# Optimization experiments

Measured on AMD Instinct MI355X. Metric: run time of the kernel, lower is better.

The kernel has to match this reference:

```python
import jax, jax.numpy as jnp
import numpy as np

B, S, D, H = 2, 2048, 1024, 16
HD = D // H  # head_dim = 64


def setup_inputs() -> dict:
    key = jax.random.key(0)
    k1, k2, k3 = jax.random.split(key, 3)
    return {
        "hidden_states": jax.random.normal(k1, (B, S, D), dtype=jnp.float32),
        "W_attn": jax.random.normal(k2, (D, 3 * D), dtype=jnp.float32) * 0.02,
        "b_attn": jnp.zeros((3 * D,), dtype=jnp.float32),
        "W_proj": jax.random.normal(k3, (D, D), dtype=jnp.float32) * 0.02,
        "b_proj": jnp.zeros((D,), dtype=jnp.float32),
    }


def reference(hidden_states, W_attn, b_attn, W_proj, b_proj):
    b, s, d = hidden_states.shape
    qkv = hidden_states @ W_attn + b_attn  # [b, s, 3d]
    q, k, v = jnp.split(qkv, 3, axis=-1)

    def split_heads(x):  # [b, s, d] -> [b, H, s, hd]
        return x.reshape(b, s, H, HD).transpose(0, 2, 1, 3)

    q, k, v = split_heads(q), split_heads(k), split_heads(v)

    # scores: [b, H, s, s]
    w = jnp.einsum("bhqd,bhkd->bhqk", q, k) / jnp.sqrt(jnp.float32(HD))
    causal = jnp.tril(jnp.ones((s, s), dtype=bool))  # [s, s]
    mask_value = jnp.finfo(w.dtype).min
    w = jnp.where(causal[None, None, :, :], w, mask_value)
    w = jax.nn.softmax(w, axis=-1)

    score = jnp.einsum("bhqk,bhkd->bhqd", w, v)  # [b, H, s, hd]
    score = score.transpose(0, 2, 1, 3).reshape(b, s, d)
    out = score @ W_proj + b_proj
    return out
```

## Files before the change

kernel.cpp:

```cpp
#include <hip/hip_runtime.h>
#include <hip/hip_bf16.h>

typedef unsigned short bf16_t;
typedef __attribute__((ext_vector_type(8))) short bf16x8;
typedef __attribute__((ext_vector_type(4))) float f32x4;

#define MFMA16(a, b, c) __builtin_amdgcn_mfma_f32_16x16x32_bf16((a), (b), (c), 0, 0, 0)

__device__ __forceinline__ bf16_t f2bf(float f) {
  union { float f; unsigned u; } v; v.f = f;
  unsigned u = v.u;
  u += 0x7FFFu + ((u >> 16) & 1u);
  return (bf16_t)(u >> 16);
}

__device__ __forceinline__ unsigned cvt_pk_bf16(float lo, float hi) {
  unsigned r;
  asm volatile("v_cvt_pk_bf16_f32 %0, %1, %2" : "=v"(r) : "v"(lo), "v"(hi));
  return r;
}

__device__ __forceinline__ void gld_lds16(const void* g, void* l) {
  __builtin_amdgcn_global_load_lds(
      (const __attribute__((address_space(1))) unsigned int*)g,
      (__attribute__((address_space(3))) unsigned int*)l, 16, 0, 0);
}

__global__ __launch_bounds__(256) void k_f32_to_bf16(const float* __restrict__ in,
                                                     bf16_t* __restrict__ out, int n8) {
  int i = blockIdx.x * 256 + threadIdx.x;
  if (i >= n8) return;
  const float4* p = (const float4*)in + (size_t)i * 2;
  float4 a = p[0], b = p[1];
  bf16x8 o;
  o[0] = (short)f2bf(a.x); o[1] = (short)f2bf(a.y); o[2] = (short)f2bf(a.z); o[3] = (short)f2bf(a.w);
  o[4] = (short)f2bf(b.x); o[5] = (short)f2bf(b.y); o[6] = (short)f2bf(b.z); o[7] = (short)f2bf(b.w);
  *((bf16x8*)out + i) = o;
}

__global__ __launch_bounds__(256) void k_transpose_bf16(const float* __restrict__ W,
                                                        bf16_t* __restrict__ Wt, int K, int N) {
  __shared__ bf16_t t[64][65];
  int n0 = blockIdx.x * 64, k0 = blockIdx.y * 64;
  int tid = threadIdx.x;
#pragma unroll
  for (int p = 0; p < 16; ++p) {
    int lin = p * 256 + tid;
    int r = lin >> 6, c = lin & 63;
    t[r][c] = f2bf(W[(size_t)(k0 + r) * N + n0 + c]);
  }
  __syncthreads();
#pragma unroll
  for (int p = 0; p < 16; ++p) {
    int lin = p * 256 + tid;
    int nr = lin >> 6, kc = lin & 63;
    Wt[(size_t)(n0 + nr) * K + k0 + kc] = t[kc][nr];
  }
}

template <bool BF16OUT, bool SCALEQ>
__global__ __launch_bounds__(256) void k_gemm_bt(const bf16_t* __restrict__ A,
                                                 const bf16_t* __restrict__ Bt,
                                                 const float* __restrict__ bias,
                                                 void* __restrict__ Cout, int M, int N, int K,
                                                 int nx) {
  __shared__ bf16_t Al[128 * 32];
  __shared__ bf16_t Bl[128 * 32];
  const int tid = threadIdx.x;
  const int lane = tid & 63;
  const int wid = tid >> 6;
  const int wm = wid >> 1, wn = wid & 1;
  const int nwg = gridDim.x;
  const int cpx = nwg >> 3;
  const int swz = (blockIdx.x & 7) * cpx + (blockIdx.x >> 3);
  const int m0 = (swz / nx) * 128, n0 = (swz % nx) * 128;
  const int lr = lane & 15;
  const int lk = lane >> 4;

  f32x4 acc[4][4] = {};

  for (int k0 = 0; k0 < K; k0 += 32) {
    __syncthreads();
#pragma unroll
    for (int p = 0; p < 2; ++p) {
      int o = p * 4096 + tid * 16;
      int row = o >> 6, cb = o & 63;
      gld_lds16((const char*)A + ((size_t)(m0 + row) * K + k0) * 2 + cb, (char*)Al + o);
      gld_lds16((const char*)Bt + ((size_t)(n0 + row) * K + k0) * 2 + cb, (char*)Bl + o);
    }
    __syncthreads();
    bf16x8 af[4], bfr[4];
#pragma unroll
    for (int i = 0; i < 4; ++i) {
      af[i]  = *(const bf16x8*)(Al + ((wm * 64 + i * 16 + lr) * 32 + lk * 8));
      bfr[i] = *(const bf16x8*)(Bl + ((wn * 64 + i * 16 + lr) * 32 + lk * 8));
    }
#pragma unroll
    for (int i = 0; i < 4; ++i)
#pragma unroll
      for (int j = 0; j < 4; ++j)
        acc[i][j] = MFMA16(af[i], bfr[j], acc[i][j]);
  }

#pragma unroll
  for (int i = 0; i < 4; ++i) {
    int grow = m0 + wm * 64 + i * 16 + lk * 4;
#pragma unroll
    for (int j = 0; j < 4; ++j) {
      int gcol = n0 + wn * 64 + j * 16 + lr;
      float bv = bias[gcol];
      float scl = (SCALEQ && gcol < 1024) ? 0.18033688011112042f : 1.0f;
#pragma unroll
      for (int r = 0; r < 4; ++r) {
        float v = (acc[i][j][r] + bv) * scl;
        size_t off = (size_t)(grow + r) * N + gcol;
        if (BF16OUT)
          ((bf16_t*)Cout)[off] = f2bf(v);
        else
          ((float*)Cout)[off] = v;
      }
    }
  }
}

__global__ __launch_bounds__(256) void k_attn(const bf16_t* __restrict__ qkv,
                                              bf16_t* __restrict__ score) {
  __shared__ bf16_t Kl[2][64 * 64];
  __shared__ bf16_t Vt[2][64 * 64];
  __shared__ bf16_t Pl[4][16 * 64];
  const int tid = threadIdx.x;
  const int lane = tid & 63;
  const int w = tid >> 6;
  const int lr = lane & 15, lk = lane >> 4;

  const int flat = blockIdx.x;
  const int qt = 31 - (flat >> 5);
  const int bh = flat & 31;
  const int b = bh >> 4, h = bh & 15;

  const bf16_t* Qb = qkv + (size_t)b * 2048 * 3072 + h * 64;
  const bf16_t* Kb = Qb + 1024;
  const bf16_t* Vb = Qb + 2048;

  int vkv[2], vd0[2], krow[2], kchk[2];
#pragma unroll
  for (int p = 0; p < 2; ++p) {
    int e = (p * 256 + tid) * 8;
    vkv[p] = e >> 6;
    vd0[p] = e & 63;
    int t2 = p * 256 + tid;
    krow[p] = t2 >> 3;
    kchk[p] = (t2 & 7) ^ (krow[p] & 7);
  }

  const int qr0 = qt * 64 + w * 16;
  const int q = qr0 + lr;
  const int jtEnd = qt + 1;

  bf16x8 qf[2];
#pragma unroll
  for (int ks = 0; ks < 2; ++ks)
    qf[ks] = *(const bf16x8*)(Qb + (size_t)(qr0 + lr) * 3072 + ks * 32 + lk * 8);

  f32x4 o[4] = {};
  float l = 0.f;

  {
    bf16x8 v0[2];
#pragma unroll
    for (int p = 0; p < 2; ++p)
      v0[p] = *(const bf16x8*)(Vb + (size_t)vkv[p] * 3072 + vd0[p]);
#pragma unroll
    for (int p = 0; p < 2; ++p)
#pragma unroll
      for (int j = 0; j < 8; ++j) {
        int d = vd0[p] + j;
        int addr = (d * 128 + vkv[p] * 2) ^ (((d & 7) ^ ((d >> 3) & 7)) << 4);
        *(bf16_t*)((char*)Vt + addr) = (bf16_t)v0[p][j];
      }
  }
  bf16x8 vrA[2], vrB[2];
#pragma unroll
  for (int p = 0; p < 2; ++p)
    vrA[p] = *(const bf16x8*)(Vb + (size_t)(64 + vkv[p]) * 3072 + vd0[p]);
#pragma unroll
  for (int p = 0; p < 2; ++p)
    gld_lds16((const char*)Kb + ((size_t)krow[p] * 3072 + kchk[p] * 8) * 2,
              (char*)Kl + (p * 256 + tid) * 16);

  auto STEP = [&](int jt, bf16x8 (&vrC)[2], bf16x8 (&vrN)[2], bool last) {
    const int kv0 = jt * 64;
    asm volatile("s_waitcnt lgkmcnt(0)" ::: "memory");
    __builtin_amdgcn_s_barrier();
    char* wbase = (char*)Vt + (((jt + 1) & 1) << 13);
#pragma unroll
    for (int p = 0; p < 2; ++p)
#pragma unroll
      for (int j = 0; j < 8; ++j) {
        int d = vd0[p] + j;
        int addr = (d * 128 + vkv[p] * 2) ^ (((d & 7) ^ ((d >> 3) & 7)) << 4);
        *(bf16_t*)(wbase + addr) = (bf16_t)vrC[p][j];
      }
    if (!last) {
      const int kvV = (kv0 + 128 < 2048) ? kv0 + 128 : 1920;
#pragma unroll
      for (int p = 0; p < 2; ++p)
        vrN[p] = *(const bf16x8*)(Vb + (size_t)(kvV + vkv[p]) * 3072 + vd0[p]);
      char* kbase = (char*)Kl + (((jt + 1) & 1) << 13);
#pragma unroll
      for (int p = 0; p < 2; ++p)
        gld_lds16((const char*)Kb + ((size_t)(kv0 + 64 + krow[p]) * 3072 + kchk[p] * 8) * 2,
                  kbase + (p * 256 + tid) * 16);
      asm volatile("s_waitcnt vmcnt(4)" ::: "memory");
    } else {
      asm volatile("s_waitcnt vmcnt(0)" ::: "memory");
    }
    const char* kread = (const char*)Kl + ((jt & 1) << 13);
    bf16x8 kf[4][2];
#pragma unroll
    for (int nc = 0; nc < 4; ++nc) {
      const char* rowp = kread + (nc * 16 + lr) * 128;
      kf[nc][0] = *(const bf16x8*)(rowp + ((lk ^ (lr & 7)) << 4));
      kf[nc][1] = *(const bf16x8*)(rowp + (((4 | lk) ^ (lr & 7)) << 4));
    }
    f32x4 s[4];
    __builtin_amdgcn_s_setprio(1);
#pragma unroll
    for (int nc = 0; nc < 4; ++nc) {
      f32x4 z = {};
      z = MFMA16(kf[nc][0], qf[0], z);
      z = MFMA16(kf[nc][1], qf[1], z);
      s[nc] = z;
    }
    __builtin_amdgcn_s_setprio(0);
    if (kv0 + 63 > qr0) {
#pragma unroll
      for (int nc = 0; nc < 4; ++nc)
#pragma unroll
        for (int r = 0; r < 4; ++r) {
          int kvi = kv0 + nc * 16 + lk * 4 + r;
          if (kvi > q) s[nc][r] = -INFINITY;
        }
    }
#pragma unroll
    for (int nc = 0; nc < 4; ++nc)
#pragma unroll
      for (int r = 0; r < 4; ++r) {
        float p = exp2f(s[nc][r]);
        s[nc][r] = p;
        l += p;
      }
    bf16_t* Pw = Pl[w];
#pragma unroll
    for (int nc = 0; nc < 4; ++nc)
#pragma unroll
      for (int r = 0; r < 4; r += 2) {
        unsigned u = cvt_pk_bf16(s[nc][r], s[nc][r + 1]);
        int addr = (lr * 128 + (nc * 16 + lk * 4 + r) * 2) ^ ((lr & 7) << 4);
        *(unsigned*)((char*)Pw + addr) = u;
      }
    const char* rbase = (const char*)Vt + ((jt & 1) << 13);
    bf16x8 pa[2];
#pragma unroll
    for (int ks = 0; ks < 2; ++ks) {
      int addr = (lr * 128 + ks * 64 + lk * 16) ^ ((lr & 7) << 4);
      pa[ks] = *(const bf16x8*)((const char*)Pl[w] + addr);
    }
    __builtin_amdgcn_s_setprio(1);
#pragma unroll
    for (int db = 0; db < 4; ++db)
#pragma unroll
      for (int ks = 0; ks < 2; ++ks) {
        int d = db * 16 + lr;
        int addr = (d * 128 + ks * 64 + lk * 16) ^ (((d & 7) ^ ((d >> 3) & 7)) << 4);
        bf16x8 vb = *(const bf16x8*)(rbase + addr);
        o[db] = MFMA16(vb, pa[ks], o[db]);
      }
    __builtin_amdgcn_s_setprio(0);
  };

  int jt = 0;
  for (;;) {
    STEP(jt, vrA, vrB, jt + 1 == jtEnd);
    if (++jt == jtEnd) break;
    STEP(jt, vrB, vrA, jt + 1 == jtEnd);
    if (++jt == jtEnd) break;
  }

  l += __shfl_xor(l, 16);
  l += __shfl_xor(l, 32);
  const float rl = 1.0f / l;
  bf16_t* orow = score + (size_t)(b * 2048 + q) * 1024 + h * 64 + lk * 4;
#pragma unroll
  for (int db = 0; db < 4; ++db) {
    unsigned w0 = cvt_pk_bf16(o[db][0] * rl, o[db][1] * rl);
    unsigned w1 = cvt_pk_bf16(o[db][2] * rl, o[db][3] * rl);
    uint2 pkt; pkt.x = w0; pkt.y = w1;
    *(uint2*)(orow + db * 16) = pkt;
  }
}

extern "C" void kernel_launch(void* const* d_in, const int* in_sizes, int n_in,
                              void* d_out, int out_size, void* d_ws, size_t ws_size,
                              hipStream_t stream) {
  const float* X  = (const float*)d_in[0];
  const float* Wa = (const float*)d_in[1];
  const float* ba = (const float*)d_in[2];
  const float* Wp = (const float*)d_in[3];
  const float* bp = (const float*)d_in[4];
  float* out = (float*)d_out;

  char* ws = (char*)d_ws;
  bf16_t* Xb  = (bf16_t*)ws;
  bf16_t* WaT = (bf16_t*)(ws + (size_t)(8u << 20));
  bf16_t* WpT = (bf16_t*)(ws + (size_t)(14u << 20));
  bf16_t* QKV = (bf16_t*)(ws + (size_t)(16u << 20));
  bf16_t* S_  = Xb;

  k_f32_to_bf16<<<2048, 256, 0, stream>>>(X, Xb, 4096 * 1024 / 8);
  k_transpose_bf16<<<dim3(48, 16), 256, 0, stream>>>(Wa, WaT, 1024, 3072);
  k_transpose_bf16<<<dim3(16, 16), 256, 0, stream>>>(Wp, WpT, 1024, 1024);
  k_gemm_bt<true, true><<<768, 256, 0, stream>>>(Xb, WaT, ba, QKV, 4096, 3072, 1024, 24);
  k_attn<<<1024, 256, 0, stream>>>(QKV, S_);
  k_gemm_bt<false, false><<<256, 256, 0, stream>>>(S_, WpT, bp, out, 4096, 1024, 1024, 8);
}
```

Measured before the change: 124.2 us.

## Narrow output-projection GEMM tiles and vectorize V transpose and P stores

The GEMM kernel now takes the N-tile width as a template parameter. The output projection uses 128x64 tiles over 512 workgroups instead of 256, so more of the GPU's compute units have work. In the attention kernel, each thread now loads V as two 4-element rows and writes packed 32-bit pairs into the transposed LDS buffer instead of 16-bit scalar writes, and the vmcnt wait is adjusted to match. P tile stores are also combined into 64-bit writes. Narrower GEMM tiles reload the A tile more often and give each workgroup less work to reuse it against.

```diff
diff --git a/kernel.cpp b/kernel.cpp
--- a/kernel.cpp
+++ b/kernel.cpp
@@ -3,6 +3,7 @@
 
 typedef unsigned short bf16_t;
 typedef __attribute__((ext_vector_type(8))) short bf16x8;
+typedef __attribute__((ext_vector_type(4))) short bf16x4;
 typedef __attribute__((ext_vector_type(4))) float f32x4;
 
 #define MFMA16(a, b, c) __builtin_amdgcn_mfma_f32_16x16x32_bf16((a), (b), (c), 0, 0, 0)
@@ -18,6 +19,10 @@
   unsigned r;
   asm volatile("v_cvt_pk_bf16_f32 %0, %1, %2" : "=v"(r) : "v"(lo), "v"(hi));
   return r;
+}
+
+__device__ __forceinline__ unsigned pack2(short lo, short hi) {
+  return ((unsigned)(unsigned short)lo) | ((unsigned)(unsigned short)hi << 16);
 }
 
 __device__ __forceinline__ void gld_lds16(const void* g, void* l) {
@@ -58,14 +63,15 @@
   }
 }
 
-template <bool BF16OUT, bool SCALEQ>
+template <bool BF16OUT, bool SCALEQ, int BN>
 __global__ __launch_bounds__(256) void k_gemm_bt(const bf16_t* __restrict__ A,
                                                  const bf16_t* __restrict__ Bt,
                                                  const float* __restrict__ bias,
                                                  void* __restrict__ Cout, int M, int N, int K,
                                                  int nx) {
+  constexpr int NJ = BN / 32;
   __shared__ bf16_t Al[128 * 32];
-  __shared__ bf16_t Bl[128 * 32];
+  __shared__ bf16_t Bl[BN * 32];
   const int tid = threadIdx.x;
   const int lane = tid & 63;
   const int wid = tid >> 6;
@@ -73,11 +79,11 @@
   const int nwg = gridDim.x;
   const int cpx = nwg >> 3;
   const int swz = (blockIdx.x & 7) * cpx + (blockIdx.x >> 3);
-  const int m0 = (swz / nx) * 128, n0 = (swz % nx) * 128;
+  const int m0 = (swz / nx) * 128, n0 = (swz % nx) * BN;
   const int lr = lane & 15;
   const int lk = lane >> 4;
 
-  f32x4 acc[4][4] = {};
+  f32x4 acc[4][NJ] = {};
 
   for (int k0 = 0; k0 < K; k0 += 32) {
     __syncthreads();
@@ -86,19 +92,25 @@
       int o = p * 4096 + tid * 16;
       int row = o >> 6, cb = o & 63;
       gld_lds16((const char*)A + ((size_t)(m0 + row) * K + k0) * 2 + cb, (char*)Al + o);
+    }
+#pragma unroll
+    for (int p = 0; p < BN / 64; ++p) {
+      int o = p * 4096 + tid * 16;
+      int row = o >> 6, cb = o & 63;
       gld_lds16((const char*)Bt + ((size_t)(n0 + row) * K + k0) * 2 + cb, (char*)Bl + o);
     }
     __syncthreads();
-    bf16x8 af[4], bfr[4];
-#pragma unroll
-    for (int i = 0; i < 4; ++i) {
-      af[i]  = *(const bf16x8*)(Al + ((wm * 64 + i * 16 + lr) * 32 + lk * 8));
-      bfr[i] = *(const bf16x8*)(Bl + ((wn * 64 + i * 16 + lr) * 32 + lk * 8));
-    }
+    bf16x8 af[4], bfr[NJ];
 #pragma unroll
     for (int i = 0; i < 4; ++i)
-#pragma unroll
-      for (int j = 0; j < 4; ++j)
+      af[i] = *(const bf16x8*)(Al + ((wm * 64 + i * 16 + lr) * 32 + lk * 8));
+#pragma unroll
+    for (int j = 0; j < NJ; ++j)
+      bfr[j] = *(const bf16x8*)(Bl + ((wn * (BN / 2) + j * 16 + lr) * 32 + lk * 8));
+#pragma unroll
+    for (int i = 0; i < 4; ++i)
+#pragma unroll
+      for (int j = 0; j < NJ; ++j)
         acc[i][j] = MFMA16(af[i], bfr[j], acc[i][j]);
   }
 
@@ -106,8 +118,8 @@
   for (int i = 0; i < 4; ++i) {
     int grow = m0 + wm * 64 + i * 16 + lk * 4;
 #pragma unroll
-    for (int j = 0; j < 4; ++j) {
-      int gcol = n0 + wn * 64 + j * 16 + lr;
+    for (int j = 0; j < NJ; ++j) {
+      int gcol = n0 + wn * (BN / 2) + j * 16 + lr;
       float bv = bias[gcol];
       float scl = (SCALEQ && gcol < 1024) ? 0.18033688011112042f : 1.0f;
 #pragma unroll
@@ -142,15 +154,14 @@
   const bf16_t* Kb = Qb + 1024;
   const bf16_t* Vb = Qb + 2048;
 
-  int vkv[2], vd0[2], krow[2], kchk[2];
+  int d0c[2], kv2[2], krow[2], kchk[2];
 #pragma unroll
   for (int p = 0; p < 2; ++p) {
-    int e = (p * 256 + tid) * 8;
-    vkv[p] = e >> 6;
-    vd0[p] = e & 63;
-    int t2 = p * 256 + tid;
-    krow[p] = t2 >> 3;
-    kchk[p] = (t2 & 7) ^ (krow[p] & 7);
+    int e = p * 256 + tid;
+    d0c[p] = (e & 15) * 4;
+    kv2[p] = (e >> 4) * 2;
+    krow[p] = e >> 3;
+    kchk[p] = (e & 7) ^ (krow[p] & 7);
   }
 
   const int qr0 = qt * 64 + w * 16;
@@ -166,29 +177,33 @@
   float l = 0.f;
 
   {
-    bf16x8 v0[2];
+    bf16x4 v0[2][2];
+#pragma unroll
+    for (int p = 0; p < 2; ++p) {
+      v0[p][0] = *(const bf16x4*)(Vb + (size_t)kv2[p] * 3072 + d0c[p]);
+      v0[p][1] = *(const bf16x4*)(Vb + (size_t)(kv2[p] + 1) * 3072 + d0c[p]);
+    }
 #pragma unroll
     for (int p = 0; p < 2; ++p)
-      v0[p] = *(const bf16x8*)(Vb + (size_t)vkv[p] * 3072 + vd0[p]);
-#pragma unroll
-    for (int p = 0; p < 2; ++p)
-#pragma unroll
-      for (int j = 0; j < 8; ++j) {
-        int d = vd0[p] + j;
-        int addr = (d * 128 + vkv[p] * 2) ^ (((d & 7) ^ ((d >> 3) & 7)) << 4);
-        *(bf16_t*)((char*)Vt + addr) = (bf16_t)v0[p][j];
-      }
-  }
-  bf16x8 vrA[2], vrB[2];
-#pragma unroll
-  for (int p = 0; p < 2; ++p)
-    vrA[p] = *(const bf16x8*)(Vb + (size_t)(64 + vkv[p]) * 3072 + vd0[p]);
+#pragma unroll
+      for (int j = 0; j < 4; ++j) {
+        int d = d0c[p] + j;
+        int addr = (d * 128 + kv2[p] * 2) ^ (((d & 7) ^ ((d >> 3) & 7)) << 4);
+        *(unsigned*)((char*)Vt + addr) = pack2(v0[p][0][j], v0[p][1][j]);
+      }
+  }
+  bf16x4 vrA[2][2], vrB[2][2];
+#pragma unroll
+  for (int p = 0; p < 2; ++p) {
+    vrA[p][0] = *(const bf16x4*)(Vb + (size_t)(64 + kv2[p]) * 3072 + d0c[p]);
+    vrA[p][1] = *(const bf16x4*)(Vb + (size_t)(64 + kv2[p] + 1) * 3072 + d0c[p]);
+  }
 #pragma unroll
   for (int p = 0; p < 2; ++p)
     gld_lds16((const char*)Kb + ((size_t)krow[p] * 3072 + kchk[p] * 8) * 2,
               (char*)Kl + (p * 256 + tid) * 16);
 
-  auto STEP = [&](int jt, bf16x8 (&vrC)[2], bf16x8 (&vrN)[2], bool last) {
+  auto STEP = [&](int jt, bf16x4 (&vrC)[2][2], bf16x4 (&vrN)[2][2], bool last) {
     const int kv0 = jt * 64;
     asm volatile("s_waitcnt lgkmcnt(0)" ::: "memory");
     __builtin_amdgcn_s_barrier();
@@ -196,22 +211,24 @@
 #pragma unroll
     for (int p = 0; p < 2; ++p)
 #pragma unroll
-      for (int j = 0; j < 8; ++j) {
-        int d = vd0[p] + j;
-        int addr = (d * 128 + vkv[p] * 2) ^ (((d & 7) ^ ((d >> 3) & 7)) << 4);
-        *(bf16_t*)(wbase + addr) = (bf16_t)vrC[p][j];
+      for (int j = 0; j < 4; ++j) {
+        int d = d0c[p] + j;
+        int addr = (d * 128 + kv2[p] * 2) ^ (((d & 7) ^ ((d >> 3) & 7)) << 4);
+        *(unsigned*)(wbase + addr) = pack2(vrC[p][0][j], vrC[p][1][j]);
       }
     if (!last) {
       const int kvV = (kv0 + 128 < 2048) ? kv0 + 128 : 1920;
 #pragma unroll
-      for (int p = 0; p < 2; ++p)
-        vrN[p] = *(const bf16x8*)(Vb + (size_t)(kvV + vkv[p]) * 3072 + vd0[p]);
+      for (int p = 0; p < 2; ++p) {
+        vrN[p][0] = *(const bf16x4*)(Vb + (size_t)(kvV + kv2[p]) * 3072 + d0c[p]);
+        vrN[p][1] = *(const bf16x4*)(Vb + (size_t)(kvV + kv2[p] + 1) * 3072 + d0c[p]);
+      }
       char* kbase = (char*)Kl + (((jt + 1) & 1) << 13);
 #pragma unroll
       for (int p = 0; p < 2; ++p)
         gld_lds16((const char*)Kb + ((size_t)(kv0 + 64 + krow[p]) * 3072 + kchk[p] * 8) * 2,
                   kbase + (p * 256 + tid) * 16);
-      asm volatile("s_waitcnt vmcnt(4)" ::: "memory");
+      asm volatile("s_waitcnt vmcnt(6)" ::: "memory");
     } else {
       asm volatile("s_waitcnt vmcnt(0)" ::: "memory");
     }
@@ -252,13 +269,13 @@
       }
     bf16_t* Pw = Pl[w];
 #pragma unroll
-    for (int nc = 0; nc < 4; ++nc)
-#pragma unroll
-      for (int r = 0; r < 4; r += 2) {
-        unsigned u = cvt_pk_bf16(s[nc][r], s[nc][r + 1]);
-        int addr = (lr * 128 + (nc * 16 + lk * 4 + r) * 2) ^ ((lr & 7) << 4);
-        *(unsigned*)((char*)Pw + addr) = u;
-      }
+    for (int nc = 0; nc < 4; ++nc) {
+      uint2 u;
+      u.x = cvt_pk_bf16(s[nc][0], s[nc][1]);
+      u.y = cvt_pk_bf16(s[nc][2], s[nc][3]);
+      int addr = (lr * 128 + (nc * 16 + lk * 4) * 2) ^ ((lr & 7) << 4);
+      *(uint2*)((char*)Pw + addr) = u;
+    }
     const char* rbase = (const char*)Vt + ((jt & 1) << 13);
     bf16x8 pa[2];
 #pragma unroll
@@ -320,7 +337,7 @@
   k_f32_to_bf16<<<2048, 256, 0, stream>>>(X, Xb, 4096 * 1024 / 8);
   k_transpose_bf16<<<dim3(48, 16), 256, 0, stream>>>(Wa, WaT, 1024, 3072);
   k_transpose_bf16<<<dim3(16, 16), 256, 0, stream>>>(Wp, WpT, 1024, 1024);
-  k_gemm_bt<true, true><<<768, 256, 0, stream>>>(Xb, WaT, ba, QKV, 4096, 3072, 1024, 24);
+  k_gemm_bt<true, true, 128><<<768, 256, 0, stream>>>(Xb, WaT, ba, QKV, 4096, 3072, 1024, 24);
   k_attn<<<1024, 256, 0, stream>>>(QKV, S_);
-  k_gemm_bt<false, false><<<256, 256, 0, stream>>>(S_, WpT, bp, out, 4096, 1024, 1024, 8);
-}
+  k_gemm_bt<false, false, 64><<<512, 256, 0, stream>>>(S_, WpT, bp, out, 4096, 1024, 1024, 16);
+}
```

Result: faster. 119.7 us (-3.6%).
